# Optimization experiments

Measured on AMD Instinct MI355X. Metric: run time of the kernel, lower is better.

## Reference

```python
import jax, jax.numpy as jnp
import numpy as np

B, N, D = 32, 2048, 512
K = 64          # cluster_size
G = 16          # ghost_clusters
BN_EPS = 1e-5
L2_EPS = 1e-12


def setup_inputs() -> dict:
    key = jax.random.key(0)
    k1, k2, k3 = jax.random.split(key, 3)
    init_sc = 1.0 / np.sqrt(D)
    x = jax.random.normal(k1, (B, N, D), dtype=jnp.float32)
    clusters = init_sc * jax.random.normal(k2, (D, K + G), dtype=jnp.float32)
    clusters2 = init_sc * jax.random.normal(k3, (D, K), dtype=jnp.float32)
    bn_gamma = jnp.ones((K + G,), dtype=jnp.float32)
    bn_beta = jnp.zeros((K + G,), dtype=jnp.float32)
    return {"x": x, "clusters": clusters, "clusters2": clusters2,
            "bn_gamma": bn_gamma, "bn_beta": bn_beta}


def _l2norm(v, axis):
    n = jnp.sqrt(jnp.sum(v * v, axis=axis, keepdims=True))
    return v / jnp.maximum(n, L2_EPS)


def reference(x, clusters, clusters2, bn_gamma, bn_beta):
    b, n, d = x.shape
    kc = clusters2.shape[1]
    # projection: [B*N, K+G]
    a = x.reshape(-1, d) @ clusters
    # BatchNorm1d (training mode: batch statistics, biased variance)
    mean = jnp.mean(a, axis=0)
    var = jnp.mean((a - mean) ** 2, axis=0)
    a = (a - mean) * jax.lax.rsqrt(var + BN_EPS) * bn_gamma + bn_beta
    # softmax over all clusters, drop ghost clusters
    a = jax.nn.softmax(a, axis=1)[:, :kc].reshape(b, n, kc)
    # fused VLAD: v[b,d,k] = sum_n a[b,n,k] * (x[b,n,d] - c2[d,k])
    a_sum = jnp.sum(a, axis=1)                              # [B, K]
    vlad = jnp.einsum('bnd,bnk->bdk', x, a)                 # [B, D, K]
    vlad = vlad - clusters2[None, :, :] * a_sum[:, None, :]
    # intra-normalize over D, flatten, global L2 normalize
    vlad = _l2norm(vlad, axis=1)
    vlad = vlad.reshape(b, kc * d)
    vlad = _l2norm(vlad, axis=1)
    return vlad
```

## Files before the change

kernel.cpp:

```cpp
#include <hip/hip_runtime.h>
#include <hip/hip_bf16.h>

#define B_ 32
#define N_ 2048
#define D_ 512
#define KC_ 64
#define KG_ 80
#define M_ (B_*N_)

typedef __attribute__((ext_vector_type(8))) short short8;
typedef __attribute__((ext_vector_type(4))) float f32x4;

__device__ __forceinline__ unsigned short bf_rn(float f){
  unsigned int u = __float_as_uint(f);
  unsigned int r = u + 0x7FFFu + ((u >> 16) & 1u);
  return (unsigned short)(r >> 16);
}
__device__ __forceinline__ float bf_up(unsigned short h){
  return __uint_as_float(((unsigned int)h) << 16);
}
__device__ __forceinline__ void cvt8(const float* v, short8& hi, short8& lo){
#pragma unroll
  for (int i=0;i<8;i++){
    unsigned short h = bf_rn(v[i]);
    float rem = v[i] - bf_up(h);
    hi[i] = (short)h;
    lo[i] = (short)bf_rn(rem);
  }
}

__global__ __launch_bounds__(256) void k0_prep(const float* __restrict__ cl,
                                               unsigned short* __restrict__ Bf)
{
  int tid = blockIdx.x*256 + threadIdx.x;
  int l  = tid & 63;
  int hl = (tid >> 6) & 1;
  int j  = (tid >> 7) % 5;
  int c  = tid / 640;
  int kk  = c*32 + (l>>4)*8;
  int col = j*16 + (l&15);
  unsigned short o[8];
#pragma unroll
  for (int jj=0;jj<8;jj++){
    float v = cl[(size_t)(kk+jj)*KG_ + col];
    unsigned short h = bf_rn(v);
    if (hl == 0) o[jj] = h;
    else         o[jj] = bf_rn(v - bf_up(h));
  }
#pragma unroll
  for (int jj=0;jj<8;jj++) Bf[(size_t)tid*8 + jj] = o[jj];
}

__global__ __launch_bounds__(256) void k1_proj(
    const float* __restrict__ x, const unsigned short* __restrict__ Bf,
    float* __restrict__ a, float* __restrict__ S1, float* __restrict__ S2)
{
  __shared__ float ls1[KG_], ls2[KG_];
  const int t = threadIdx.x;
  const int w = t >> 6, lane = t & 63;
  const int m = lane & 15, q = lane >> 4;
  const int row0 = blockIdx.x*128 + w*32;
  if (t < KG_){ ls1[t]=0.f; ls2[t]=0.f; }

  const float* xr0 = x + (size_t)(row0 + m)*D_ + q*8;
  const float* xr1 = xr0 + (size_t)16*D_;

  f32x4 acc[2][5];
#pragma unroll
  for (int rt=0;rt<2;rt++)
#pragma unroll
    for (int j=0;j<5;j++) acc[rt][j] = (f32x4){0.f,0.f,0.f,0.f};

  for (int c=0;c<16;c++){
    float v0[8], v1[8];
    *(float4*)&v0[0] = *(const float4*)(xr0 + c*32);
    *(float4*)&v0[4] = *(const float4*)(xr0 + c*32 + 4);
    *(float4*)&v1[0] = *(const float4*)(xr1 + c*32);
    *(float4*)&v1[4] = *(const float4*)(xr1 + c*32 + 4);
    short8 ah0, al0, ah1, al1;
    cvt8(v0, ah0, al0);
    cvt8(v1, ah1, al1);
    const unsigned short* bp = Bf + (size_t)(c*5)*1024 + lane*8;
#pragma unroll
    for (int j=0;j<5;j++){
      short8 bhi = *(const short8*)(bp + (size_t)j*1024);
      short8 blo = *(const short8*)(bp + (size_t)j*1024 + 512);
      acc[0][j] = __builtin_amdgcn_mfma_f32_16x16x32_bf16(ah0, bhi, acc[0][j], 0,0,0);
      acc[0][j] = __builtin_amdgcn_mfma_f32_16x16x32_bf16(al0, bhi, acc[0][j], 0,0,0);
      acc[0][j] = __builtin_amdgcn_mfma_f32_16x16x32_bf16(ah0, blo, acc[0][j], 0,0,0);
      acc[1][j] = __builtin_amdgcn_mfma_f32_16x16x32_bf16(ah1, bhi, acc[1][j], 0,0,0);
      acc[1][j] = __builtin_amdgcn_mfma_f32_16x16x32_bf16(al1, bhi, acc[1][j], 0,0,0);
      acc[1][j] = __builtin_amdgcn_mfma_f32_16x16x32_bf16(ah1, blo, acc[1][j], 0,0,0);
    }
  }

  float s1v[5] = {0,0,0,0,0}, s2v[5] = {0,0,0,0,0};
#pragma unroll
  for (int rt=0;rt<2;rt++){
#pragma unroll
    for (int j=0;j<5;j++){
      f32x4 v = acc[rt][j];
      size_t base = (size_t)(row0 + rt*16 + q*4)*KG_ + j*16 + m;
      a[base]        = v[0];
      a[base+KG_]    = v[1];
      a[base+2*KG_]  = v[2];
      a[base+3*KG_]  = v[3];
      s1v[j] += v[0]+v[1]+v[2]+v[3];
      s2v[j] += v[0]*v[0]+v[1]*v[1]+v[2]*v[2]+v[3]*v[3];
    }
  }
#pragma unroll
  for (int j=0;j<5;j++){
    float s1 = s1v[j], s2 = s2v[j];
    s1 += __shfl_xor(s1,16); s1 += __shfl_xor(s1,32);
    s2 += __shfl_xor(s2,16); s2 += __shfl_xor(s2,32);
    if (q == 0){
      atomicAdd(&ls1[j*16+m], s1);
      atomicAdd(&ls2[j*16+m], s2);
    }
  }
  __syncthreads();
  if (t < KG_){ atomicAdd(&S1[t], ls1[t]); atomicAdd(&S2[t], ls2[t]); }
}

__global__ void k2_bn(const float* __restrict__ S1, const float* __restrict__ S2,
                      const float* __restrict__ gamma, const float* __restrict__ beta,
                      float* __restrict__ scale, float* __restrict__ shift)
{
  int t = threadIdx.x;
  if (t < KG_){
    const float invM = 1.0f / (float)M_;
    float mean = S1[t] * invM;
    float var  = S2[t] * invM - mean*mean;
    float sc = gamma[t] * rsqrtf(var + 1e-5f);
    scale[t] = sc;
    shift[t] = beta[t] - mean*sc;
  }
}

__global__ __launch_bounds__(256) void k3_softmax(
    float* __restrict__ a, const float* __restrict__ scale,
    const float* __restrict__ shift, float* __restrict__ asum)
{
  __shared__ float as[64*84];
  __shared__ float sc[KG_], sh[KG_];
  __shared__ float lsum[KC_];
  const int t = threadIdx.x;
  const int row0 = blockIdx.x * 64;
  if (t < KG_){ sc[t]=scale[t]; sh[t]=shift[t]; }
  if (t < KC_) lsum[t]=0.f;
  __syncthreads();
#pragma unroll
  for (int l=0;l<20;l++){
    int idx = t + 256*l;
    int r = idx/80, col = idx - r*80;
    float v = a[(size_t)(row0+r)*KG_ + col];
    as[r*84+col] = v*sc[col] + sh[col];
  }
  __syncthreads();
  const int rt = t >> 2;
  const int g  = t & 3;
  float m = -1e30f;
#pragma unroll
  for (int c=0;c<20;c++) m = fmaxf(m, as[rt*84 + g + 4*c]);
  m = fmaxf(m, __shfl_xor(m,1));
  m = fmaxf(m, __shfl_xor(m,2));
  float e[20]; float s = 0.f;
#pragma unroll
  for (int c=0;c<20;c++){ float v = __expf(as[rt*84 + g + 4*c] - m); e[c]=v; s+=v; }
  s += __shfl_xor(s,1);
  s += __shfl_xor(s,2);
  const float inv = 1.f/s;
#pragma unroll
  for (int c=0;c<16;c++){
    int col = g + 4*c;
    float pv = e[c]*inv;
    a[(size_t)(row0+rt)*KG_ + col] = pv;
    float su = pv;
    su += __shfl_xor(su,4);  su += __shfl_xor(su,8);
    su += __shfl_xor(su,16); su += __shfl_xor(su,32);
    if ((t&63) < 4) atomicAdd(&lsum[col], su);
  }
  __syncthreads();
  if (t < KC_) atomicAdd(&asum[(blockIdx.x>>5)*KC_ + t], lsum[t]);
}

__global__ __launch_bounds__(256) void k4_vlad(
    const float* __restrict__ x, const float* __restrict__ p, float* __restrict__ vp)
{
  __shared__ unsigned short xh[64*40], xl[64*40];
  __shared__ unsigned short ph[64*40], pl[64*40];
  const int t = threadIdx.x;
  const int blk = blockIdx.x;
  const int ns = blk & 3;
  const int dt = (blk >> 2) & 7;
  const int b  = blk >> 5;
  const int w = t >> 6, lane = t & 63;
  const int m = lane & 15, q = lane >> 4;
  const int d0 = dt*64;
  const int nbase = ns*512;
  const int dloc = t & 63, ng = t >> 6;

  f32x4 acc[4];
#pragma unroll
  for (int j=0;j<4;j++) acc[j] = (f32x4){0.f,0.f,0.f,0.f};

  for (int n0=0;n0<512;n0+=32){
    {
      float v[8];
      const float* xp = x + ((size_t)b*N_ + nbase + n0 + ng*8)*D_ + d0 + dloc;
#pragma unroll
      for (int jj=0;jj<8;jj++) v[jj] = xp[(size_t)jj*D_];
      short8 hi, lo; cvt8(v, hi, lo);
      *(short8*)&xh[dloc*40 + ng*8] = hi;
      *(short8*)&xl[dloc*40 + ng*8] = lo;
    }
    {
      float v[8];
      const float* pp = p + ((size_t)b*N_ + nbase + n0 + ng*8)*KG_ + dloc;
#pragma unroll
      for (int jj=0;jj<8;jj++) v[jj] = pp[(size_t)jj*KG_];
      short8 hi, lo; cvt8(v, hi, lo);
      *(short8*)&ph[dloc*40 + ng*8] = hi;
      *(short8*)&pl[dloc*40 + ng*8] = lo;
    }
    __syncthreads();
    short8 ahi = *(const short8*)&xh[(w*16+m)*40 + q*8];
    short8 alo = *(const short8*)&xl[(w*16+m)*40 + q*8];
#pragma unroll
    for (int j=0;j<4;j++){
      short8 bhi = *(const short8*)&ph[(j*16+m)*40 + q*8];
      short8 blo = *(const short8*)&pl[(j*16+m)*40 + q*8];
      acc[j] = __builtin_amdgcn_mfma_f32_16x16x32_bf16(ahi, bhi, acc[j], 0,0,0);
      acc[j] = __builtin_amdgcn_mfma_f32_16x16x32_bf16(alo, bhi, acc[j], 0,0,0);
      acc[j] = __builtin_amdgcn_mfma_f32_16x16x32_bf16(ahi, blo, acc[j], 0,0,0);
    }
    __syncthreads();
  }
#pragma unroll
  for (int j=0;j<4;j++){
    f32x4 v = acc[j];
    size_t base = (((size_t)ns*B_ + b)*D_ + d0 + w*16 + q*4)*KC_ + j*16 + m;
    vp[base]         = v[0];
    vp[base +   KC_] = v[1];
    vp[base + 2*KC_] = v[2];
    vp[base + 3*KC_] = v[3];
  }
}

__global__ __launch_bounds__(1024) void k5_norm(
    const float* __restrict__ vp, const float* __restrict__ c2,
    const float* __restrict__ asum, float* __restrict__ out)
{
  __shared__ float part[16][64];
  __shared__ float invd[64];
  __shared__ float gi_s;
  const int b = blockIdx.x;
  const int t = threadIdx.x;
  const int k = t & 63, dg = t >> 6;
  const float av = asum[b*KC_ + k];
  const size_t stride = (size_t)B_*D_*KC_;
  float v[32];
  float ss = 0.f;
#pragma unroll
  for (int s=0;s<32;s++){
    int d = dg + 16*s;
    size_t idx = ((size_t)b*D_ + d)*KC_ + k;
    float vv = 0.f;
#pragma unroll
    for (int nsp=0;nsp<4;nsp++) vv += vp[idx + (size_t)nsp*stride];
    vv -= c2[d*KC_ + k]*av;
    v[s] = vv;
    ss += vv*vv;
  }
  part[dg][k] = ss;
  __syncthreads();
  if (t < 64){
    float n2 = 0.f;
#pragma unroll
    for (int i=0;i<16;i++) n2 += part[i][t];
    float nn = sqrtf(n2);
    float denom = fmaxf(nn, 1e-12f);
    invd[t] = 1.f/denom;
    float ratio = nn/denom;
    float r2 = ratio*ratio;
#pragma unroll
    for (int mm=1;mm<64;mm<<=1) r2 += __shfl_xor(r2, mm);
    if (t==0){
      float g = sqrtf(r2);
      gi_s = 1.f/fmaxf(g, 1e-12f);
    }
  }
  __syncthreads();
  const float gi = gi_s;
  const float ik = invd[k];
#pragma unroll
  for (int s=0;s<32;s++){
    int d = dg + 16*s;
    out[(size_t)b*(D_*KC_) + (size_t)d*KC_ + k] = v[s]*ik*gi;
  }
}

extern "C" void kernel_launch(void* const* d_in, const int* in_sizes, int n_in,
                              void* d_out, int out_size, void* d_ws, size_t ws_size,
                              hipStream_t stream)
{
  const float* x     = (const float*)d_in[0];
  const float* cl    = (const float*)d_in[1];
  const float* c2    = (const float*)d_in[2];
  const float* gamma = (const float*)d_in[3];
  const float* beta  = (const float*)d_in[4];
  float* out = (float*)d_out;
  float* ws  = (float*)d_ws;

  float* S1    = ws;
  float* S2    = ws + 80;
  float* scale = ws + 160;
  float* shift = ws + 240;
  float* asum  = ws + 320;
  unsigned short* Bf = (unsigned short*)(ws + 4096);
  float* a     = ws + 45056;
  float* vp    = a + (size_t)M_*KG_;

  hipMemsetAsync(ws, 0, 2368*sizeof(float), stream);
  k0_prep   <<<40,   256, 0, stream>>>(cl, Bf);
  k1_proj   <<<512,  256, 0, stream>>>(x, Bf, a, S1, S2);
  k2_bn     <<<1,    128, 0, stream>>>(S1, S2, gamma, beta, scale, shift);
  k3_softmax<<<1024, 256, 0, stream>>>(a, scale, shift, asum);
  k4_vlad   <<<1024, 256, 0, stream>>>(x, a, vp);
  k5_norm   <<<32,  1024, 0, stream>>>(vp, c2, asum, out);
}
```

Baseline: 274.9 us.

## Double-buffer VLAD smem tiles and pre-split softmax output into bf16 hi/lo

The softmax kernel now stores each probability as a packed bf16 hi/lo pair in a 32-bit word, so the VLAD kernel no longer has to convert assignments. The VLAD kernel double-buffers its shared-memory tiles and prefetches the next chunk from global memory while the current chunk's MFMAs run, which halves the barriers per iteration. Each thread's loads now follow the MFMA operand layout, so the tile can be stored directly without padded transposes. It also adds a launch-bounds occupancy hint. Global loads are now 16-wide strided per quarter-wave rather than 64-wide, which may lower coalescing, and the doubled LDS footprint could limit occupancy.

```diff
diff --git a/kernel.cpp b/kernel.cpp
--- a/kernel.cpp
+++ b/kernel.cpp
@@ -145,6 +145,7 @@
   __shared__ float as[64*84];
   __shared__ float sc[KG_], sh[KG_];
   __shared__ float lsum[KC_];
+  unsigned int* p32 = (unsigned int*)a;
   const int t = threadIdx.x;
   const int row0 = blockIdx.x * 64;
   if (t < KG_){ sc[t]=scale[t]; sh[t]=shift[t]; }
@@ -175,7 +176,9 @@
   for (int c=0;c<16;c++){
     int col = g + 4*c;
     float pv = e[c]*inv;
-    a[(size_t)(row0+rt)*KG_ + col] = pv;
+    unsigned short h = bf_rn(pv);
+    unsigned short lo = bf_rn(pv - bf_up(h));
+    p32[(size_t)(row0+rt)*KG_ + col] = (unsigned int)h | ((unsigned int)lo << 16);
     float su = pv;
     su += __shfl_xor(su,4);  su += __shfl_xor(su,8);
     su += __shfl_xor(su,16); su += __shfl_xor(su,32);
@@ -185,11 +188,12 @@
   if (t < KC_) atomicAdd(&asum[(blockIdx.x>>5)*KC_ + t], lsum[t]);
 }
 
-__global__ __launch_bounds__(256) void k4_vlad(
-    const float* __restrict__ x, const float* __restrict__ p, float* __restrict__ vp)
-{
-  __shared__ unsigned short xh[64*40], xl[64*40];
-  __shared__ unsigned short ph[64*40], pl[64*40];
+__global__ __launch_bounds__(256,4) void k4_vlad(
+    const float* __restrict__ x, const unsigned int* __restrict__ p32,
+    float* __restrict__ vp)
+{
+  __shared__ unsigned short xh[2][2048], xl[2][2048];
+  __shared__ unsigned short ph[2][2048], pl[2][2048];
   const int t = threadIdx.x;
   const int blk = blockIdx.x;
   const int ns = blk & 3;
@@ -199,52 +203,71 @@
   const int m = lane & 15, q = lane >> 4;
   const int d0 = dt*64;
   const int nbase = ns*512;
-  const int dloc = t & 63, ng = t >> 6;
+
+  const float*        xbase = x   + ((size_t)b*N_ + nbase + q*8)*D_  + d0 + w*16 + m;
+  const unsigned int* pbase = p32 + ((size_t)b*N_ + nbase + q*8)*KG_ + w*16 + m;
 
   f32x4 acc[4];
 #pragma unroll
   for (int j=0;j<4;j++) acc[j] = (f32x4){0.f,0.f,0.f,0.f};
 
-  for (int n0=0;n0<512;n0+=32){
-    {
-      float v[8];
-      const float* xp = x + ((size_t)b*N_ + nbase + n0 + ng*8)*D_ + d0 + dloc;
+  float v[8]; unsigned int u[8];
+#pragma unroll
+  for (int jj=0;jj<8;jj++) v[jj] = xbase[(size_t)jj*D_];
+#pragma unroll
+  for (int jj=0;jj<8;jj++) u[jj] = pbase[(size_t)jj*KG_];
+  {
+    short8 hi, lo; cvt8(v, hi, lo);
+    *(short8*)&xh[0][t*8] = hi;
+    *(short8*)&xl[0][t*8] = lo;
+    short8 hp, lp;
+#pragma unroll
+    for (int jj=0;jj<8;jj++){ hp[jj] = (short)(u[jj] & 0xFFFFu); lp[jj] = (short)(u[jj] >> 16); }
+    *(short8*)&ph[0][t*8] = hp;
+    *(short8*)&pl[0][t*8] = lp;
+  }
+
+  int cur = 0;
+  for (int c=0;c<16;c++){
+    __syncthreads();
+    if (c < 15){
+      const float*        xp = xbase + (size_t)(c+1)*32*D_;
+      const unsigned int* pp = pbase + (size_t)(c+1)*32*KG_;
 #pragma unroll
       for (int jj=0;jj<8;jj++) v[jj] = xp[(size_t)jj*D_];
-      short8 hi, lo; cvt8(v, hi, lo);
-      *(short8*)&xh[dloc*40 + ng*8] = hi;
-      *(short8*)&xl[dloc*40 + ng*8] = lo;
-    }
-    {
-      float v[8];
-      const float* pp = p + ((size_t)b*N_ + nbase + n0 + ng*8)*KG_ + dloc;
-#pragma unroll
-      for (int jj=0;jj<8;jj++) v[jj] = pp[(size_t)jj*KG_];
-      short8 hi, lo; cvt8(v, hi, lo);
-      *(short8*)&ph[dloc*40 + ng*8] = hi;
-      *(short8*)&pl[dloc*40 + ng*8] = lo;
-    }
-    __syncthreads();
-    short8 ahi = *(const short8*)&xh[(w*16+m)*40 + q*8];
-    short8 alo = *(const short8*)&xl[(w*16+m)*40 + q*8];
+#pragma unroll
+      for (int jj=0;jj<8;jj++) u[jj] = pp[(size_t)jj*KG_];
+    }
+    short8 ahi = *(const short8*)&xh[cur][(w*64+lane)*8];
+    short8 alo = *(const short8*)&xl[cur][(w*64+lane)*8];
 #pragma unroll
     for (int j=0;j<4;j++){
-      short8 bhi = *(const short8*)&ph[(j*16+m)*40 + q*8];
-      short8 blo = *(const short8*)&pl[(j*16+m)*40 + q*8];
+      short8 bhi = *(const short8*)&ph[cur][(j*64+lane)*8];
+      short8 blo = *(const short8*)&pl[cur][(j*64+lane)*8];
       acc[j] = __builtin_amdgcn_mfma_f32_16x16x32_bf16(ahi, bhi, acc[j], 0,0,0);
       acc[j] = __builtin_amdgcn_mfma_f32_16x16x32_bf16(alo, bhi, acc[j], 0,0,0);
       acc[j] = __builtin_amdgcn_mfma_f32_16x16x32_bf16(ahi, blo, acc[j], 0,0,0);
     }
-    __syncthreads();
+    if (c < 15){
+      short8 hi, lo; cvt8(v, hi, lo);
+      *(short8*)&xh[cur^1][t*8] = hi;
+      *(short8*)&xl[cur^1][t*8] = lo;
+      short8 hp, lp;
+#pragma unroll
+      for (int jj=0;jj<8;jj++){ hp[jj] = (short)(u[jj] & 0xFFFFu); lp[jj] = (short)(u[jj] >> 16); }
+      *(short8*)&ph[cur^1][t*8] = hp;
+      *(short8*)&pl[cur^1][t*8] = lp;
+    }
+    cur ^= 1;
   }
 #pragma unroll
   for (int j=0;j<4;j++){
-    f32x4 v = acc[j];
+    f32x4 vv = acc[j];
     size_t base = (((size_t)ns*B_ + b)*D_ + d0 + w*16 + q*4)*KC_ + j*16 + m;
-    vp[base]         = v[0];
-    vp[base +   KC_] = v[1];
-    vp[base + 2*KC_] = v[2];
-    vp[base + 3*KC_] = v[3];
+    vp[base]         = vv[0];
+    vp[base +   KC_] = vv[1];
+    vp[base + 2*KC_] = vv[2];
+    vp[base + 3*KC_] = vv[3];
   }
 }
 
@@ -327,6 +350,6 @@
   k1_proj   <<<512,  256, 0, stream>>>(x, Bf, a, S1, S2);
   k2_bn     <<<1,    128, 0, stream>>>(S1, S2, gamma, beta, scale, shift);
   k3_softmax<<<1024, 256, 0, stream>>>(a, scale, shift, asum);
-  k4_vlad   <<<1024, 256, 0, stream>>>(x, a, vp);
+  k4_vlad   <<<1024, 256, 0, stream>>>(x, (const unsigned int*)a, vp);
   k5_norm   <<<32,  1024, 0, stream>>>(vp, c2, asum, out);
 }
```

After: 275.5 us. No clear change (+0.2%).
